# Kernel tuning notes

Hardware: AMD Instinct MI355X
Metric: run time of the kernel (lower is better)

The kernel has to match this reference:

```python
import jax, jax.numpy as jnp
import numpy as np

TEMPERATURE = 0.05
EPS = 1e-8  # F.cosine_similarity default eps


def setup_inputs() -> dict:
    key = jax.random.key(0)
    k1, k2 = jax.random.split(key)
    N, D = 8192, 256
    return {
        "query_embeddings": jax.random.normal(k1, (N, D), dtype=jnp.float32),
        "pos_embeddings": jax.random.normal(k2, (N, D), dtype=jnp.float32),
    }


def _normalize(x):
    # matches F.cosine_similarity: x / max(||x||, eps)
    norm = jnp.sqrt(jnp.sum(x * x, axis=-1, keepdims=True))
    return x / jnp.maximum(norm, EPS)


def reference(query_embeddings, pos_embeddings):
    q = _normalize(query_embeddings)  # [N, D]
    p = _normalize(pos_embeddings)    # [N, D]
    # cosine similarity matrix via GEMM instead of (N,N,D) broadcast
    sim = jnp.einsum("nd,md->nm", q, p) / TEMPERATURE  # [N, N]
    # cross-entropy with labels = arange(N): loss_i = logsumexp(sim_i) - sim_ii
    logz = jax.nn.logsumexp(sim, axis=-1)  # [N]
    diag = jnp.diagonal(sim)               # [N]
    loss = jnp.mean(logz - diag)
    return loss
```

## Files before the change

kernel.cpp:

```cpp
#include <hip/hip_runtime.h>
#include <hip/hip_bf16.h>

#define NROWS 8192
#define DDIM  256
#define INV_TEMP 20.0f

typedef __attribute__((ext_vector_type(8))) short bf16x8;
typedef __attribute__((ext_vector_type(4))) float f32x4;

__device__ static inline void async16(const void* g, void* l) {
    __builtin_amdgcn_global_load_lds(
        (const __attribute__((address_space(1))) void*)g,
        (__attribute__((address_space(3))) void*)l, 16, 0, 0);
}

__global__ __launch_bounds__(64) void norm_diag_kernel(
    const float* __restrict__ q, const float* __restrict__ p,
    unsigned short* __restrict__ qn, unsigned short* __restrict__ pn,
    float* __restrict__ diag)
{
    const int row  = blockIdx.x;
    const int lane = threadIdx.x;

    const float4 qv = ((const float4*)(q + (size_t)row * DDIM))[lane];
    const float4 pv = ((const float4*)(p + (size_t)row * DDIM))[lane];

    float sq = qv.x*qv.x + qv.y*qv.y + qv.z*qv.z + qv.w*qv.w;
    float sp = pv.x*pv.x + pv.y*pv.y + pv.z*pv.z + pv.w*pv.w;
    #pragma unroll
    for (int m = 1; m < 64; m <<= 1) {
        sq += __shfl_xor(sq, m);
        sp += __shfl_xor(sp, m);
    }
    const float qs = 1.0f / fmaxf(sqrtf(sq), 1e-8f);
    const float ps = 1.0f / fmaxf(sqrtf(sp), 1e-8f);

    const float qx = qv.x*qs, qy = qv.y*qs, qz = qv.z*qs, qw = qv.w*qs;
    const float px = pv.x*ps, py = pv.y*ps, pz = pv.z*ps, pw = pv.w*ps;

    float d = qx*px + qy*py + qz*pz + qw*pw;
    #pragma unroll
    for (int m = 1; m < 64; m <<= 1) d += __shfl_xor(d, m);
    if (lane == 0) diag[row] = d * INV_TEMP;

    union { unsigned short u16[4]; uint2 v; } uq, up;
    {
        __hip_bfloat16 b;
        b = __float2bfloat16(qx); uq.u16[0] = *(unsigned short*)&b;
        b = __float2bfloat16(qy); uq.u16[1] = *(unsigned short*)&b;
        b = __float2bfloat16(qz); uq.u16[2] = *(unsigned short*)&b;
        b = __float2bfloat16(qw); uq.u16[3] = *(unsigned short*)&b;
        b = __float2bfloat16(px); up.u16[0] = *(unsigned short*)&b;
        b = __float2bfloat16(py); up.u16[1] = *(unsigned short*)&b;
        b = __float2bfloat16(pz); up.u16[2] = *(unsigned short*)&b;
        b = __float2bfloat16(pw); up.u16[3] = *(unsigned short*)&b;
    }
    *(uint2*)(qn + (size_t)row * DDIM + lane * 4) = uq.v;
    *(uint2*)(pn + (size_t)row * DDIM + lane * 4) = up.v;
}

__global__ __launch_bounds__(256, 2) void simexp_kernel(
    const unsigned short* __restrict__ qn,
    const unsigned short* __restrict__ pn,
    float* __restrict__ part)
{
    __shared__ unsigned char lds[16384];

    const int tid  = threadIdx.x;
    const int lane = tid & 63;
    const int w    = tid >> 6;
    const int wr   = w >> 1;
    const int wc   = w & 1;
    const int quad = lane >> 4;
    const int l16  = lane & 15;
    const int rowbase = blockIdx.y * 128;
    const int colbase = blockIdx.x * 128;

    const unsigned short* gA0 = qn + (size_t)(rowbase + (2*w  )*16 + l16) * DDIM + quad * 8;
    const unsigned short* gA1 = qn + (size_t)(rowbase + (2*w+1)*16 + l16) * DDIM + quad * 8;
    const unsigned short* gB0 = pn + (size_t)(colbase + (2*w  )*16 + l16) * DDIM + quad * 8;
    const unsigned short* gB1 = pn + (size_t)(colbase + (2*w+1)*16 + l16) * DDIM + quad * 8;

    unsigned char* ldsA = lds;
    unsigned char* ldsB = lds + 8192;

    f32x4 acc[4][4];
    #pragma unroll
    for (int i = 0; i < 4; ++i)
        #pragma unroll
        for (int j = 0; j < 4; ++j) acc[i][j] = (f32x4)0.0f;

    for (int ks = 0; ks < 8; ++ks) {
        __syncthreads();
        async16(gA0 + ks * 32, ldsA + (2*w    ) * 1024);
        async16(gA1 + ks * 32, ldsA + (2*w + 1) * 1024);
        async16(gB0 + ks * 32, ldsB + (2*w    ) * 1024);
        async16(gB1 + ks * 32, ldsB + (2*w + 1) * 1024);
        __syncthreads();

        bf16x8 af[4], bf[4];
        #pragma unroll
        for (int i = 0; i < 4; ++i)
            af[i] = *(const bf16x8*)(ldsA + (wr*4 + i) * 1024 + quad * 256 + l16 * 16);
        #pragma unroll
        for (int j = 0; j < 4; ++j)
            bf[j] = *(const bf16x8*)(ldsB + (wc*4 + j) * 1024 + quad * 256 + l16 * 16);

        #pragma unroll
        for (int i = 0; i < 4; ++i)
            #pragma unroll
            for (int j = 0; j < 4; ++j)
                acc[i][j] = __builtin_amdgcn_mfma_f32_16x16x32_bf16(
                    af[i], bf[j], acc[i][j], 0, 0, 0);
    }

    __syncthreads();
    float* red = (float*)lds;

    #pragma unroll
    for (int i = 0; i < 4; ++i)
        #pragma unroll
        for (int r = 0; r < 4; ++r) {
            float s = __expf(acc[i][0][r] * INV_TEMP)
                    + __expf(acc[i][1][r] * INV_TEMP)
                    + __expf(acc[i][2][r] * INV_TEMP)
                    + __expf(acc[i][3][r] * INV_TEMP);
            s += __shfl_xor(s, 1);
            s += __shfl_xor(s, 2);
            s += __shfl_xor(s, 4);
            s += __shfl_xor(s, 8);
            if (l16 == 0)
                red[wc * 128 + wr * 64 + i * 16 + quad * 4 + r] = s;
        }
    __syncthreads();

    if (tid < 128)
        part[(size_t)blockIdx.x * NROWS + rowbase + tid] = red[tid] + red[128 + tid];
}

__global__ __launch_bounds__(128) void rowsum_kernel(
    const float* __restrict__ part, const float* __restrict__ diag,
    float* __restrict__ loss_part)
{
    const int row = blockIdx.x * 128 + threadIdx.x;
    float s = 0.0f;
    #pragma unroll 4
    for (int cb = 0; cb < 64; ++cb)
        s += part[(size_t)cb * NROWS + row];
    float v = logf(s) - diag[row];

    #pragma unroll
    for (int m = 1; m < 64; m <<= 1) v += __shfl_xor(v, m);
    __shared__ float wsum[2];
    if ((threadIdx.x & 63) == 0) wsum[threadIdx.x >> 6] = v;
    __syncthreads();
    if (threadIdx.x == 0) loss_part[blockIdx.x] = wsum[0] + wsum[1];
}

__global__ __launch_bounds__(64) void final_kernel(
    const float* __restrict__ loss_part, float* __restrict__ out)
{
    float v = loss_part[threadIdx.x];
    #pragma unroll
    for (int m = 1; m < 64; m <<= 1) v += __shfl_xor(v, m);
    if (threadIdx.x == 0) out[0] = v * (1.0f / NROWS);
}

extern "C" void kernel_launch(void* const* d_in, const int* in_sizes, int n_in,
                              void* d_out, int out_size, void* d_ws, size_t ws_size,
                              hipStream_t stream)
{
    const float* q = (const float*)d_in[0];
    const float* p = (const float*)d_in[1];

    char* ws = (char*)d_ws;
    unsigned short* qn   = (unsigned short*)ws;
    unsigned short* pn   = (unsigned short*)(ws + (size_t)NROWS*DDIM*2);
    float* part      = (float*)(ws + 2*(size_t)NROWS*DDIM*2);
    float* diag      = part + 64 * (size_t)NROWS;
    float* loss_part = diag + NROWS;

    norm_diag_kernel<<<NROWS, 64, 0, stream>>>(q, p, qn, pn, diag);

    dim3 grid(64, 64);
    simexp_kernel<<<grid, 256, 0, stream>>>(qn, pn, part);

    rowsum_kernel<<<64, 128, 0, stream>>>(part, diag, loss_part);
    final_kernel<<<1, 64, 0, stream>>>(loss_part, (float*)d_out);
}
```

Baseline: 146.1 us.

## Triple-buffer LDS loads in simexp GEMM and pack four rows per norm block

The similarity GEMM now uses a three-stage LDS ring buffer. Async global-to-LDS loads for step k+2 are issued before computing step k, with explicit vmcnt waits and barriers replacing the two syncthreads per iteration. This overlaps memory latency with MFMA work, but LDS per block grows to 48KB, which may cap occupancy despite the launch bound raised to 3. Separately, the normalization kernel processes four rows per 256-thread block instead of one row per 64-thread block, cutting block count and launch overhead.

```diff
diff --git a/kernel.cpp b/kernel.cpp
--- a/kernel.cpp
+++ b/kernel.cpp
@@ -14,13 +14,13 @@
         (__attribute__((address_space(3))) void*)l, 16, 0, 0);
 }
 
-__global__ __launch_bounds__(64) void norm_diag_kernel(
+__global__ __launch_bounds__(256) void norm_diag_kernel(
     const float* __restrict__ q, const float* __restrict__ p,
     unsigned short* __restrict__ qn, unsigned short* __restrict__ pn,
     float* __restrict__ diag)
 {
-    const int row  = blockIdx.x;
-    const int lane = threadIdx.x;
+    const int row  = (blockIdx.x << 2) + (threadIdx.x >> 6);
+    const int lane = threadIdx.x & 63;
 
     const float4 qv = ((const float4*)(q + (size_t)row * DDIM))[lane];
     const float4 pv = ((const float4*)(p + (size_t)row * DDIM))[lane];
@@ -59,12 +59,12 @@
     *(uint2*)(pn + (size_t)row * DDIM + lane * 4) = up.v;
 }
 
-__global__ __launch_bounds__(256, 2) void simexp_kernel(
+__global__ __launch_bounds__(256, 3) void simexp_kernel(
     const unsigned short* __restrict__ qn,
     const unsigned short* __restrict__ pn,
     float* __restrict__ part)
 {
-    __shared__ unsigned char lds[16384];
+    __shared__ unsigned char lds[3 * 16384];
 
     const int tid  = threadIdx.x;
     const int lane = tid & 63;
@@ -81,30 +81,38 @@
     const unsigned short* gB0 = pn + (size_t)(colbase + (2*w  )*16 + l16) * DDIM + quad * 8;
     const unsigned short* gB1 = pn + (size_t)(colbase + (2*w+1)*16 + l16) * DDIM + quad * 8;
 
-    unsigned char* ldsA = lds;
-    unsigned char* ldsB = lds + 8192;
-
     f32x4 acc[4][4];
     #pragma unroll
     for (int i = 0; i < 4; ++i)
         #pragma unroll
         for (int j = 0; j < 4; ++j) acc[i][j] = (f32x4)0.0f;
 
+#define STAGE(buf, ks) do {                                             \
+        unsigned char* _b = lds + (buf) * 16384;                        \
+        async16(gA0 + (ks) * 32, _b +        (2*w    ) * 1024);         \
+        async16(gA1 + (ks) * 32, _b +        (2*w + 1) * 1024);         \
+        async16(gB0 + (ks) * 32, _b + 8192 + (2*w    ) * 1024);         \
+        async16(gB1 + (ks) * 32, _b + 8192 + (2*w + 1) * 1024);         \
+    } while (0)
+
+    STAGE(0, 0);
+    STAGE(1, 1);
+    asm volatile("s_waitcnt vmcnt(4)" ::: "memory");
+    __builtin_amdgcn_s_barrier();
+    asm volatile("" ::: "memory");
+
+    #pragma unroll
     for (int ks = 0; ks < 8; ++ks) {
-        __syncthreads();
-        async16(gA0 + ks * 32, ldsA + (2*w    ) * 1024);
-        async16(gA1 + ks * 32, ldsA + (2*w + 1) * 1024);
-        async16(gB0 + ks * 32, ldsB + (2*w    ) * 1024);
-        async16(gB1 + ks * 32, ldsB + (2*w + 1) * 1024);
-        __syncthreads();
-
+        if (ks < 6) STAGE((ks + 2) % 3, ks + 2);
+
+        const unsigned char* ba = lds + (ks % 3) * 16384;
         bf16x8 af[4], bf[4];
         #pragma unroll
         for (int i = 0; i < 4; ++i)
-            af[i] = *(const bf16x8*)(ldsA + (wr*4 + i) * 1024 + quad * 256 + l16 * 16);
+            af[i] = *(const bf16x8*)(ba + (wr*4 + i) * 1024 + quad * 256 + l16 * 16);
         #pragma unroll
         for (int j = 0; j < 4; ++j)
-            bf[j] = *(const bf16x8*)(ldsB + (wc*4 + j) * 1024 + quad * 256 + l16 * 16);
+            bf[j] = *(const bf16x8*)(ba + 8192 + (wc*4 + j) * 1024 + quad * 256 + l16 * 16);
 
         #pragma unroll
         for (int i = 0; i < 4; ++i)
@@ -112,7 +120,15 @@
             for (int j = 0; j < 4; ++j)
                 acc[i][j] = __builtin_amdgcn_mfma_f32_16x16x32_bf16(
                     af[i], bf[j], acc[i][j], 0, 0, 0);
+
+        if (ks < 7) {
+            if (ks < 6) { asm volatile("s_waitcnt vmcnt(4)" ::: "memory"); }
+            else        { asm volatile("s_waitcnt vmcnt(0)" ::: "memory"); }
+            __builtin_amdgcn_s_barrier();
+            asm volatile("" ::: "memory");
+        }
     }
+#undef STAGE
 
     __syncthreads();
     float* red = (float*)lds;
@@ -180,7 +196,7 @@
     float* diag      = part + 64 * (size_t)NROWS;
     float* loss_part = diag + NROWS;
 
-    norm_diag_kernel<<<NROWS, 64, 0, stream>>>(q, p, qn, pn, diag);
+    norm_diag_kernel<<<NROWS/4, 256, 0, stream>>>(q, p, qn, pn, diag);
 
     dim3 grid(64, 64);
     simexp_kernel<<<grid, 256, 0, stream>>>(qn, pn, part);
```

After: 136.5 us. 6.6% less time.

## Load GEMM fragments directly from global into registers with double buffering

Applied to the files above, without the earlier changes.

The similarity GEMM kernel no longer stages tiles through LDS with async loads and barriers. Each wave now reads its bf16 MFMA fragments straight from global memory into registers, with a two-stage register double buffer that prefetches the next K slice. The occupancy hint is raised to 3 blocks per CU, and the normalization kernel packs 4 rows per 256-thread block. Dropping the barriers and LDS traffic trades for redundant global/L2 reads, since waves sharing a row or column tile each fetch it separately, plus extra register pressure.

```diff
diff --git a/kernel.cpp b/kernel.cpp
--- a/kernel.cpp
+++ b/kernel.cpp
@@ -8,19 +8,13 @@
 typedef __attribute__((ext_vector_type(8))) short bf16x8;
 typedef __attribute__((ext_vector_type(4))) float f32x4;
 
-__device__ static inline void async16(const void* g, void* l) {
-    __builtin_amdgcn_global_load_lds(
-        (const __attribute__((address_space(1))) void*)g,
-        (__attribute__((address_space(3))) void*)l, 16, 0, 0);
-}
-
-__global__ __launch_bounds__(64) void norm_diag_kernel(
+__global__ __launch_bounds__(256) void norm_diag_kernel(
     const float* __restrict__ q, const float* __restrict__ p,
     unsigned short* __restrict__ qn, unsigned short* __restrict__ pn,
     float* __restrict__ diag)
 {
-    const int row  = blockIdx.x;
-    const int lane = threadIdx.x;
+    const int row  = (blockIdx.x << 2) + (threadIdx.x >> 6);
+    const int lane = threadIdx.x & 63;
 
     const float4 qv = ((const float4*)(q + (size_t)row * DDIM))[lane];
     const float4 pv = ((const float4*)(p + (size_t)row * DDIM))[lane];
@@ -59,12 +53,12 @@
     *(uint2*)(pn + (size_t)row * DDIM + lane * 4) = up.v;
 }
 
-__global__ __launch_bounds__(256, 2) void simexp_kernel(
+__global__ __launch_bounds__(256, 3) void simexp_kernel(
     const unsigned short* __restrict__ qn,
     const unsigned short* __restrict__ pn,
     float* __restrict__ part)
 {
-    __shared__ unsigned char lds[16384];
+    __shared__ float red[256];
 
     const int tid  = threadIdx.x;
     const int lane = tid & 63;
@@ -76,13 +70,8 @@
     const int rowbase = blockIdx.y * 128;
     const int colbase = blockIdx.x * 128;
 
-    const unsigned short* gA0 = qn + (size_t)(rowbase + (2*w  )*16 + l16) * DDIM + quad * 8;
-    const unsigned short* gA1 = qn + (size_t)(rowbase + (2*w+1)*16 + l16) * DDIM + quad * 8;
-    const unsigned short* gB0 = pn + (size_t)(colbase + (2*w  )*16 + l16) * DDIM + quad * 8;
-    const unsigned short* gB1 = pn + (size_t)(colbase + (2*w+1)*16 + l16) * DDIM + quad * 8;
-
-    unsigned char* ldsA = lds;
-    unsigned char* ldsB = lds + 8192;
+    const unsigned short* a0 = qn + (size_t)(rowbase + wr*64 + l16) * DDIM + quad * 8;
+    const unsigned short* b0 = pn + (size_t)(colbase + wc*64 + l16) * DDIM + quad * 8;
 
     f32x4 acc[4][4];
     #pragma unroll
@@ -90,32 +79,30 @@
         #pragma unroll
         for (int j = 0; j < 4; ++j) acc[i][j] = (f32x4)0.0f;
 
+    bf16x8 af[2][4], bf[2][4];
+
+#define LOADF(buf, ks) do {                                                  \
+        _Pragma("unroll")                                                    \
+        for (int i = 0; i < 4; ++i) {                                        \
+            af[buf][i] = *(const bf16x8*)(a0 + (size_t)i * 16 * DDIM + (ks) * 32); \
+            bf[buf][i] = *(const bf16x8*)(b0 + (size_t)i * 16 * DDIM + (ks) * 32); \
+        }                                                                    \
+    } while (0)
+
+    LOADF(0, 0);
+
+    #pragma unroll
     for (int ks = 0; ks < 8; ++ks) {
-        __syncthreads();
-        async16(gA0 + ks * 32, ldsA + (2*w    ) * 1024);
-        async16(gA1 + ks * 32, ldsA + (2*w + 1) * 1024);
-        async16(gB0 + ks * 32, ldsB + (2*w    ) * 1024);
-        async16(gB1 + ks * 32, ldsB + (2*w + 1) * 1024);
-        __syncthreads();
-
-        bf16x8 af[4], bf[4];
-        #pragma unroll
-        for (int i = 0; i < 4; ++i)
-            af[i] = *(const bf16x8*)(ldsA + (wr*4 + i) * 1024 + quad * 256 + l16 * 16);
-        #pragma unroll
-        for (int j = 0; j < 4; ++j)
-            bf[j] = *(const bf16x8*)(ldsB + (wc*4 + j) * 1024 + quad * 256 + l16 * 16);
-
+        if (ks < 7) LOADF((ks + 1) & 1, ks + 1);
+        const int cur = ks & 1;
         #pragma unroll
         for (int i = 0; i < 4; ++i)
             #pragma unroll
             for (int j = 0; j < 4; ++j)
                 acc[i][j] = __builtin_amdgcn_mfma_f32_16x16x32_bf16(
-                    af[i], bf[j], acc[i][j], 0, 0, 0);
+                    af[cur][i], bf[cur][j], acc[i][j], 0, 0, 0);
     }
-
-    __syncthreads();
-    float* red = (float*)lds;
+#undef LOADF
 
     #pragma unroll
     for (int i = 0; i < 4; ++i)
@@ -180,7 +167,7 @@
     float* diag      = part + 64 * (size_t)NROWS;
     float* loss_part = diag + NROWS;
 
-    norm_diag_kernel<<<NROWS, 64, 0, stream>>>(q, p, qn, pn, diag);
+    norm_diag_kernel<<<NROWS/4, 256, 0, stream>>>(q, p, qn, pn, diag);
 
     dim3 grid(64, 64);
     simexp_kernel<<<grid, 256, 0, stream>>>(qn, pn, part);
```

Measured after the change: 199.2 us. 1.36x slower.
